# Performance work log

Measured on AMD Instinct MI355X. Metric: run time of the kernel, lower is better.

## Reference

```python
import jax, jax.numpy as jnp
import numpy as np

L, B, E = 2048, 32, 1          # seq_len, batch, embed_dim
S, D, N = 4, 8, 8              # zdim, hdim, ndim
P = 720                        # pred_len


def setup_inputs() -> dict:
    key = jax.random.key(0)
    ks = jax.random.split(key, 21)
    g = lambda i, shp, s=0.1: (jax.random.normal(ks[i], shp, dtype=jnp.float32) * s)
    return {
        'x': jax.random.normal(ks[0], (B, L, E), dtype=jnp.float32),
        'norm_w': jnp.ones((E,), jnp.float32),
        'norm_b': g(1, (E,)),
        'ema_delta': g(2, (E, N, 1), 1.0),
        'ema_alpha': g(3, (E, N, 1), 1.0),
        'ema_beta': g(4, (E, N, 1), 1.0),
        'ema_gamma': g(5, (E, N), 1.0),
        'ema_omega': g(6, (E,), 1.0),
        'Wv': g(7, (D, E)), 'bv': g(8, (D,)),
        'Wmx': g(9, (S + D + 2 * E, E)), 'bmx': g(10, (S + D + 2 * E,)),
        'Wh': g(11, (E, D)), 'bh': g(12, (E,)),
        'attn_gamma': g(13, (2, S), 1.0), 'attn_beta': g(14, (2, S), 1.0),
        'rot_alpha': g(15, (1, S), 1.0), 'rot_beta': g(16, (1, S), 1.0),
        'Wlin': g(17, (P, L), 0.02), 'blin': g(18, (P,)),
    }


def _rotary_bias(slen, a, b):
    # a, b: (1, S) learned vectors rotated per position; bias = A @ B^T (slen x slen)
    half = a.shape[-1] // 2
    freq = jnp.exp(jnp.arange(half, dtype=jnp.float32) * (-np.log(10000.0) / half))
    pos = jnp.arange(slen, dtype=jnp.float32)[:, None] * freq[None, :]  # (slen, half)
    sin, cos = jnp.sin(pos), jnp.cos(pos)

    def rot(v):  # (1, S) -> (slen, S)
        v1, v2 = v[:, :half], v[:, half:]
        return jnp.concatenate([v1 * cos - v2 * sin, v2 * cos + v1 * sin], axis=-1)

    return rot(a) @ rot(b).T  # (slen, slen)


def _forward(x, norm_w, norm_b, ema_delta, ema_alpha, ema_beta, ema_gamma, ema_omega,
             Wv, bv, Wmx, bmx, Wh, bh, attn_gamma, attn_beta, rot_alpha, rot_beta,
             Wlin, blin):
    silu = jax.nn.silu
    xs = jnp.transpose(x, (1, 0, 2))           # (L, B, E) -- torch permute(1,0,2)
    residual = xs
    # prenorm LayerNorm over embed dim
    mu = xs.mean(-1, keepdims=True)
    var = ((xs - mu) ** 2).mean(-1, keepdims=True)
    xn = norm_w * (xs - mu) * jax.lax.rsqrt(var + 1e-5) + norm_b

    v = silu(xn @ Wv.T + bv)                   # (L, B, D)

    # --- MultiHeadEMA via FFT convolution ---
    res_e = xn * ema_omega                     # (L, B, E)
    xt = jnp.transpose(xn, (1, 2, 0))          # (B, E, L)
    p = jax.nn.sigmoid(ema_delta)              # (E, N, 1)
    q = 1.0 - p * jax.nn.sigmoid(ema_alpha)
    vander = jnp.arange(L, dtype=jnp.float32)[None, None, :] * jnp.log(q)  # (E, N, L)
    kern = (p * ema_beta) * jnp.exp(vander)    # (E, N, L)
    k1d = jnp.einsum('enl,en->el', kern, ema_gamma * (1.0 / np.sqrt(N)))   # (E, L)
    kf = jnp.fft.rfft(k1d, n=2 * L)
    xf = jnp.fft.rfft(xt, n=2 * L)
    conv = jnp.fft.irfft(xf * kf, n=2 * L)[..., :L]                        # (B, E, L)
    mx = silu(jnp.transpose(conv, (2, 0, 1)) + res_e)                      # (L, B, E)

    # --- gated projections ---
    base = mx @ Wmx.T + bmx                    # (L, B, E + S + D + E)
    u = jax.nn.sigmoid(base[..., :E])          # update gate (L, B, E)
    zr = silu(base[..., E:E + S + D])
    hx = base[..., E + S + D:]                 # (L, B, E)
    z, r = zr[..., :S], zr[..., S:]            # (L,B,S), (L,B,D)
    z2 = z[..., None, :] * attn_gamma + attn_beta  # (L, B, 2, S)
    q_ = jnp.transpose(z2[..., 0, :], (1, 0, 2))   # (B, L, S)
    k_ = jnp.transpose(z2[..., 1, :], (1, 0, 2))   # (B, L, S)
    v_ = jnp.transpose(v, (1, 0, 2))               # (B, L, D)

    # --- element (relu^2) attention with rotary relative bias ---
    bias = _rotary_bias(L, rot_alpha, rot_beta)    # (L, L)
    qk = jnp.einsum('bls,bms->blm', q_, k_) / L + bias
    attn = jnp.square(jax.nn.relu(qk))             # (B, L, L)
    h = jnp.einsum('blm,bmd->bld', attn, v_)       # (B, L, D)
    h = jnp.transpose(h, (1, 0, 2))                # (L, B, D)
    h = silu(hx + (h * r) @ Wh.T + bh)             # (L, B, E)
    out = residual + u * (h - residual)            # (L, B, E)

    # trailing Linear over time axis
    y = jnp.transpose(out, (1, 2, 0)) @ Wlin.T + blin   # (B, E, P)
    return jnp.transpose(y, (0, 2, 1))                  # (B, P, E)


def reference(x, norm_w, norm_b, ema_delta, ema_alpha, ema_beta, ema_gamma, ema_omega,
              Wv, bv, Wmx, bmx, Wh, bh, attn_gamma, attn_beta, rot_alpha, rot_beta,
              Wlin, blin):
    return _forward(x, norm_w, norm_b, ema_delta, ema_alpha, ema_beta, ema_gamma,
                    ema_omega, Wv, bv, Wmx, bmx, Wh, bh, attn_gamma, attn_beta,
                    rot_alpha, rot_beta, Wlin, blin)
```

## Files before the change

kernel.cpp:

```cpp
#include <hip/hip_runtime.h>
#include <hip/hip_bf16.h>
#include <math.h>

#define LEN 2048
#define BDIM 32
#define PDIM 720

__device__ __attribute__((aligned(16))) float g_Qv[LEN * 8];
__device__ __attribute__((aligned(16))) float g_Kv[LEN * 8];
__device__ __attribute__((aligned(16))) float g_u[LEN];
__device__ __attribute__((aligned(16))) float g_hx[LEN];
__device__ __attribute__((aligned(16))) float g_wsum[LEN];
__device__ __attribute__((aligned(16))) float g_hh[LEN];

__device__ __forceinline__ float sigmoidf_(float x) { return 1.0f / (1.0f + expf(-x)); }
__device__ __forceinline__ float siluf_(float x)    { return x / (1.0f + expf(-x)); }

__global__ void k1_precompute(
    const float* __restrict__ norm_b,
    const float* __restrict__ ema_delta, const float* __restrict__ ema_alpha,
    const float* __restrict__ ema_beta,  const float* __restrict__ ema_gamma,
    const float* __restrict__ ema_omega,
    const float* __restrict__ Wv, const float* __restrict__ bv,
    const float* __restrict__ Wmx, const float* __restrict__ bmx,
    const float* __restrict__ Wh,
    const float* __restrict__ attn_gamma, const float* __restrict__ attn_beta,
    const float* __restrict__ rot_alpha,  const float* __restrict__ rot_beta)
{
    const int l = blockIdx.x * blockDim.x + threadIdx.x;
    if (l >= LEN) return;

    const float c = norm_b[0];
    const float res_e = c * ema_omega[0];

    float conv = 0.0f;
    #pragma unroll
    for (int n = 0; n < 8; ++n) {
        float p  = sigmoidf_(ema_delta[n]);
        float s  = sigmoidf_(ema_alpha[n]);
        float om = p * s;
        float q  = 1.0f - om;
        float g  = p * ema_beta[n] * ema_gamma[n] * 0.35355339059327373f;
        float qp = expf((float)(l + 1) * logf(q));
        conv += g * (1.0f - qp) / om;
    }
    conv *= c;

    const float mx = siluf_(conv + res_e);

    const float u  = sigmoidf_(fmaf(mx, Wmx[0], bmx[0]));
    float z[4];
    #pragma unroll
    for (int s = 0; s < 4; ++s) z[s] = siluf_(fmaf(mx, Wmx[1 + s], bmx[1 + s]));
    float r[8];
    #pragma unroll
    for (int d = 0; d < 8; ++d) r[d] = siluf_(fmaf(mx, Wmx[5 + d], bmx[5 + d]));
    const float hx = fmaf(mx, Wmx[13], bmx[13]);

    float ws = 0.0f;
    #pragma unroll
    for (int d = 0; d < 8; ++d) {
        float v = siluf_(fmaf(c, Wv[d], bv[d]));
        ws += v * r[d] * Wh[d];
    }

    const float f1 = expf(-logf(10000.0f) * 0.5f);
    const float c0 = cosf((float)l),      s0 = sinf((float)l);
    const float th = (float)l * f1;
    const float c1 = cosf(th),            s1 = sinf(th);

    const float ra0 = rot_alpha[0] * c0 - rot_alpha[2] * s0;
    const float ra1 = rot_alpha[1] * c1 - rot_alpha[3] * s1;
    const float ra2 = rot_alpha[2] * c0 + rot_alpha[0] * s0;
    const float ra3 = rot_alpha[3] * c1 + rot_alpha[1] * s1;
    const float rb0 = rot_beta[0] * c0 - rot_beta[2] * s0;
    const float rb1 = rot_beta[1] * c1 - rot_beta[3] * s1;
    const float rb2 = rot_beta[2] * c0 + rot_beta[0] * s0;
    const float rb3 = rot_beta[3] * c1 + rot_beta[1] * s1;

    const float invL = 1.0f / (float)LEN;
    float* q8 = g_Qv + l * 8;
    float* k8 = g_Kv + l * 8;
    #pragma unroll
    for (int s = 0; s < 4; ++s) {
        q8[s] = fmaf(z[s], attn_gamma[s],     attn_beta[s])     * invL;
        k8[s] = fmaf(z[s], attn_gamma[4 + s], attn_beta[4 + s]);
    }
    q8[4] = ra0; q8[5] = ra1; q8[6] = ra2; q8[7] = ra3;
    k8[4] = rb0; k8[5] = rb1; k8[6] = rb2; k8[7] = rb3;

    g_u[l] = u; g_hx[l] = hx; g_wsum[l] = ws;
}

__global__ void k2_rowsum(const float* __restrict__ bh)
{
    const int l = blockIdx.x;
    const int tid = threadIdx.x;

    const float* q8 = g_Qv + l * 8;
    const float q0 = q8[0], q1 = q8[1], q2 = q8[2], q3 = q8[3];
    const float q4 = q8[4], q5 = q8[5], q6 = q8[6], q7 = q8[7];

    const float4* K4 = (const float4*)g_Kv;
    float acc = 0.0f;
    #pragma unroll
    for (int k = 0; k < LEN / 256; ++k) {
        int m = tid + k * 256;
        float4 ka = K4[m * 2];
        float4 kb = K4[m * 2 + 1];
        float d = q0 * ka.x + q1 * ka.y + q2 * ka.z + q3 * ka.w
                + q4 * kb.x + q5 * kb.y + q6 * kb.z + q7 * kb.w;
        d = fmaxf(d, 0.0f);
        acc = fmaf(d, d, acc);
    }
    #pragma unroll
    for (int off = 32; off; off >>= 1) acc += __shfl_down(acc, off, 64);

    __shared__ float red[4];
    if ((tid & 63) == 0) red[tid >> 6] = acc;
    __syncthreads();
    if (tid == 0) {
        float A = red[0] + red[1] + red[2] + red[3];
        g_hh[l] = siluf_(g_hx[l] + A * g_wsum[l] + bh[0]);
    }
}

__global__ void kB_output(
    const float* __restrict__ x,
    const float* __restrict__ Wlin, const float* __restrict__ blin,
    float* __restrict__ y)
{
    const int p0    = blockIdx.x * 2;
    const int tid   = threadIdx.x;
    const int wave  = tid >> 6;
    const int lane  = tid & 63;
    const int bbase = wave * 4;

    const float4* W0 = (const float4*)(Wlin + (size_t)p0 * LEN);
    const float4* W1 = (const float4*)(Wlin + (size_t)(p0 + 1) * LEN);
    const float4* U4 = (const float4*)g_u;
    const float4* H4 = (const float4*)g_hh;

    float acc0[4] = {0, 0, 0, 0};
    float acc1[4] = {0, 0, 0, 0};

    #pragma unroll 2
    for (int k = 0; k < 8; ++k) {
        const int i4 = (k << 6) + lane;
        const float4 w0 = W0[i4];
        const float4 w1 = W1[i4];
        const float4 uv = U4[i4];
        const float4 hv = H4[i4];
        float4 xv[4];
        #pragma unroll
        for (int j = 0; j < 4; ++j)
            xv[j] = ((const float4*)(x + (size_t)(bbase + j) * LEN))[i4];

        #pragma unroll
        for (int j = 0; j < 4; ++j) {
            float ox = fmaf(uv.x, hv.x - xv[j].x, xv[j].x);
            float oy = fmaf(uv.y, hv.y - xv[j].y, xv[j].y);
            float oz = fmaf(uv.z, hv.z - xv[j].z, xv[j].z);
            float ow = fmaf(uv.w, hv.w - xv[j].w, xv[j].w);
            acc0[j] += fmaf(ox, w0.x, fmaf(oy, w0.y, fmaf(oz, w0.z, ow * w0.w)));
            acc1[j] += fmaf(ox, w1.x, fmaf(oy, w1.y, fmaf(oz, w1.z, ow * w1.w)));
        }
    }

    #pragma unroll
    for (int j = 0; j < 4; ++j) {
        float v0 = acc0[j], v1 = acc1[j];
        #pragma unroll
        for (int off = 32; off; off >>= 1) {
            v0 += __shfl_down(v0, off, 64);
            v1 += __shfl_down(v1, off, 64);
        }
        if (lane == 0) {
            const size_t row = (size_t)(bbase + j) * PDIM;
            y[row + p0]     = v0 + blin[p0];
            y[row + p0 + 1] = v1 + blin[p0 + 1];
        }
    }
}

extern "C" void kernel_launch(void* const* d_in, const int* in_sizes, int n_in,
                              void* d_out, int out_size, void* d_ws, size_t ws_size,
                              hipStream_t stream)
{
    const float* x          = (const float*)d_in[0];
    const float* norm_b     = (const float*)d_in[2];
    const float* ema_delta  = (const float*)d_in[3];
    const float* ema_alpha  = (const float*)d_in[4];
    const float* ema_beta   = (const float*)d_in[5];
    const float* ema_gamma  = (const float*)d_in[6];
    const float* ema_omega  = (const float*)d_in[7];
    const float* Wv         = (const float*)d_in[8];
    const float* bv         = (const float*)d_in[9];
    const float* Wmx        = (const float*)d_in[10];
    const float* bmx        = (const float*)d_in[11];
    const float* Wh         = (const float*)d_in[12];
    const float* bh         = (const float*)d_in[13];
    const float* attn_gamma = (const float*)d_in[14];
    const float* attn_beta  = (const float*)d_in[15];
    const float* rot_alpha  = (const float*)d_in[16];
    const float* rot_beta   = (const float*)d_in[17];
    const float* Wlin       = (const float*)d_in[18];
    const float* blin       = (const float*)d_in[19];
    float* y = (float*)d_out;

    k1_precompute<<<LEN / 256, 256, 0, stream>>>(
        norm_b, ema_delta, ema_alpha, ema_beta, ema_gamma, ema_omega,
        Wv, bv, Wmx, bmx, Wh, attn_gamma, attn_beta, rot_alpha, rot_beta);

    k2_rowsum<<<LEN, 256, 0, stream>>>(bh);

    kB_output<<<PDIM / 2, 512, 0, stream>>>(x, Wlin, blin, y);
}
```

Baseline: 121.3 us.

## Tile row-sum kernel so each block handles eight query rows against shared K

The relu-squared row-sum kernel now processes eight query rows per block instead of one. The whole K matrix (2048x8 floats, 64 KB) is staged into LDS in transposed layout, and each thread reuses every loaded K vector across eight dot products. This cuts global/L2 K traffic and block count by eight, in exchange for a large LDS footprint that limits occupancy and a staging phase per block.

After: 116.4 us. -4.0%, faster.

```diff
diff --git a/kernel.cpp b/kernel.cpp
--- a/kernel.cpp
+++ b/kernel.cpp
@@ -5,6 +5,7 @@
 #define LEN 2048
 #define BDIM 32
 #define PDIM 720
+#define LROWS 8
 
 __device__ __attribute__((aligned(16))) float g_Qv[LEN * 8];
 __device__ __attribute__((aligned(16))) float g_Kv[LEN * 8];
@@ -92,35 +93,66 @@
     g_u[l] = u; g_hx[l] = hx; g_wsum[l] = ws;
 }
 
-__global__ void k2_rowsum(const float* __restrict__ bh)
-{
-    const int l = blockIdx.x;
-    const int tid = threadIdx.x;
-
-    const float* q8 = g_Qv + l * 8;
-    const float q0 = q8[0], q1 = q8[1], q2 = q8[2], q3 = q8[3];
-    const float q4 = q8[4], q5 = q8[5], q6 = q8[6], q7 = q8[7];
-
-    const float4* K4 = (const float4*)g_Kv;
-    float acc = 0.0f;
-    #pragma unroll
-    for (int k = 0; k < LEN / 256; ++k) {
-        int m = tid + k * 256;
-        float4 ka = K4[m * 2];
-        float4 kb = K4[m * 2 + 1];
-        float d = q0 * ka.x + q1 * ka.y + q2 * ka.z + q3 * ka.w
-                + q4 * kb.x + q5 * kb.y + q6 * kb.z + q7 * kb.w;
-        d = fmaxf(d, 0.0f);
-        acc = fmaf(d, d, acc);
-    }
-    #pragma unroll
-    for (int off = 32; off; off >>= 1) acc += __shfl_down(acc, off, 64);
-
-    __shared__ float red[4];
-    if ((tid & 63) == 0) red[tid >> 6] = acc;
+__global__ void k2_tiled(const float* __restrict__ bh)
+{
+    __shared__ float kv[8][LEN];
+    __shared__ float red[4][LROWS];
+
+    const int tid   = threadIdx.x;
+    const int wave  = tid >> 6;
+    const int lane  = tid & 63;
+    const int lbase = blockIdx.x * LROWS;
+
+    #pragma unroll
+    for (int k = 0; k < 8; ++k) {
+        const int m = tid + (k << 8);
+        const float4 ka = ((const float4*)g_Kv)[m * 2];
+        const float4 kb = ((const float4*)g_Kv)[m * 2 + 1];
+        kv[0][m] = ka.x; kv[1][m] = ka.y; kv[2][m] = ka.z; kv[3][m] = ka.w;
+        kv[4][m] = kb.x; kv[5][m] = kb.y; kv[6][m] = kb.z; kv[7][m] = kb.w;
+    }
+
+    float q[LROWS][8];
+    #pragma unroll
+    for (int r = 0; r < LROWS; ++r) {
+        const float4 qa = ((const float4*)g_Qv)[(lbase + r) * 2];
+        const float4 qb = ((const float4*)g_Qv)[(lbase + r) * 2 + 1];
+        q[r][0] = qa.x; q[r][1] = qa.y; q[r][2] = qa.z; q[r][3] = qa.w;
+        q[r][4] = qb.x; q[r][5] = qb.y; q[r][6] = qb.z; q[r][7] = qb.w;
+    }
     __syncthreads();
-    if (tid == 0) {
-        float A = red[0] + red[1] + red[2] + red[3];
+
+    float acc[LROWS] = {0, 0, 0, 0, 0, 0, 0, 0};
+    #pragma unroll
+    for (int k = 0; k < 8; ++k) {
+        const int m = tid + (k << 8);
+        float kd[8];
+        #pragma unroll
+        for (int d = 0; d < 8; ++d) kd[d] = kv[d][m];
+        #pragma unroll
+        for (int r = 0; r < LROWS; ++r) {
+            float dot = q[r][0] * kd[0] + q[r][1] * kd[1] + q[r][2] * kd[2]
+                      + q[r][3] * kd[3] + q[r][4] * kd[4] + q[r][5] * kd[5]
+                      + q[r][6] * kd[6] + q[r][7] * kd[7];
+            dot = fmaxf(dot, 0.0f);
+            acc[r] = fmaf(dot, dot, acc[r]);
+        }
+    }
+
+    #pragma unroll
+    for (int r = 0; r < LROWS; ++r) {
+        #pragma unroll
+        for (int off = 32; off; off >>= 1)
+            acc[r] += __shfl_down(acc[r], off, 64);
+    }
+    if (lane == 0) {
+        #pragma unroll
+        for (int r = 0; r < LROWS; ++r) red[wave][r] = acc[r];
+    }
+    __syncthreads();
+    if (tid < LROWS) {
+        const int l = lbase + tid;
+        float A = red[0][tid] + red[1][tid] + red[2][tid] + red[3][tid];
         g_hh[l] = siluf_(g_hx[l] + A * g_wsum[l] + bh[0]);
     }
 }
@@ -212,7 +244,7 @@
         norm_b, ema_delta, ema_alpha, ema_beta, ema_gamma, ema_omega,
         Wv, bv, Wmx, bmx, Wh, attn_gamma, attn_beta, rot_alpha, rot_beta);
 
-    k2_rowsum<<<LEN, 256, 0, stream>>>(bh);
+    k2_tiled<<<LEN / LROWS, 256, 0, stream>>>(bh);
 
     kB_output<<<PDIM / 2, 512, 0, stream>>>(x, Wlin, blin, y);
 }
```
